# Performance work log

Hardware: AMD Instinct MI355X
Metric: run time of the kernel (lower is better)

The kernel has to match this reference:

```python
import jax, jax.numpy as jnp
import numpy as np

DIM = 1024
NUM_HEADS = 16
HEAD_DIM = DIM // NUM_HEADS
SCALE = HEAD_DIM ** -0.5


def rotate_half(x):
    x1, x2 = jnp.split(x, 2, axis=-1)
    return jnp.concatenate((-x2, x1), axis=-1)


def setup_inputs() -> dict:
    key = jax.random.key(0)
    ks = jax.random.split(key, 8)
    B, N = 2, 2048
    x = jax.random.normal(ks[0], (B, N, DIM), dtype=jnp.float32)
    # RoPE tables, broadcast over batch and heads
    pos = jnp.arange(N, dtype=jnp.float32)[:, None]
    inv_freq = 1.0 / (10000.0 ** (jnp.arange(0, HEAD_DIM, 2, dtype=jnp.float32) / HEAD_DIM))
    ang = pos * inv_freq[None, :]                       # [N, HEAD_DIM/2]
    ang = jnp.concatenate([ang, ang], axis=-1)          # [N, HEAD_DIM]
    rope_cos = jnp.cos(ang)[None, None]                 # [1,1,N,HEAD_DIM]
    rope_sin = jnp.sin(ang)[None, None]
    s = DIM ** -0.5
    qkv_w = jax.random.normal(ks[1], (3 * DIM, DIM), dtype=jnp.float32) * s
    qkv_b = jnp.zeros((3 * DIM,), dtype=jnp.float32)
    proj_w = jax.random.normal(ks[2], (DIM, DIM), dtype=jnp.float32) * s
    proj_b = jnp.zeros((DIM,), dtype=jnp.float32)
    return {"x": x, "rope_cos": rope_cos, "rope_sin": rope_sin,
            "qkv_w": qkv_w, "qkv_b": qkv_b, "proj_w": proj_w, "proj_b": proj_b}


def reference(x, rope_cos, rope_sin, qkv_w, qkv_b, proj_w, proj_b):
    B, N, C = x.shape
    H, D = NUM_HEADS, HEAD_DIM
    qkv = x @ qkv_w.T + qkv_b                            # [B,N,3C]
    qkv = qkv.reshape(B, N, 3, H, D).transpose(2, 0, 3, 1, 4)  # [3,B,H,N,D]
    q, k, v = qkv[0], qkv[1], qkv[2]
    # RoPE on q, k
    q = q * rope_cos + rotate_half(q) * rope_sin
    k = k * rope_cos + rotate_half(k) * rope_sin
    # scaled dot-product attention
    scores = jnp.einsum('bhnd,bhmd->bhnm', q, k) * SCALE
    attn = jax.nn.softmax(scores, axis=-1)
    out = jnp.einsum('bhnm,bhmd->bhnd', attn, v)         # [B,H,N,D]
    out = out.transpose(0, 2, 1, 3).reshape(B, N, C)
    return out @ proj_w.T + proj_b
```

## Files before the change

### kernel.cpp

```cpp
#include <hip/hip_runtime.h>
#include <hip/hip_bf16.h>

#define NUM_HEADS 16
#define HEAD_DIM 64
#define DIM 1024
#define NTOK 2048
#define MTOT 4096

typedef __attribute__((ext_vector_type(8))) short bf16x8;
typedef __attribute__((ext_vector_type(4))) float f32x4;
typedef __attribute__((ext_vector_type(16))) float f32x16;
typedef __attribute__((ext_vector_type(2))) unsigned int uint2v;

__device__ __forceinline__ unsigned short f2bf(float f) {
    union { __hip_bfloat16 h; unsigned short u; } c;
    c.h = __float2bfloat16(f);
    return c.u;
}

__device__ __forceinline__ unsigned int packbf(float lo, float hi) {
    union { unsigned short us[2]; unsigned int u; } p;
    p.us[0] = f2bf(lo); p.us[1] = f2bf(hi);
    return p.u;
}

__device__ __forceinline__ void plswap(unsigned int &a, unsigned int &b) {
#if __has_builtin(__builtin_amdgcn_permlane32_swap)
    uint2v r = __builtin_amdgcn_permlane32_swap(a, b, false, false);
    a = r[0]; b = r[1];
#else
    unsigned int pa = (unsigned int)__shfl_xor((int)a, 32);
    unsigned int pb = (unsigned int)__shfl_xor((int)b, 32);
    bool hi = (threadIdx.x & 32) != 0;
    unsigned int an = hi ? pb : a;
    unsigned int bn = hi ? b : pa;
    a = an; b = bn;
#endif
}

__device__ __forceinline__ void gload16(const unsigned short* g, unsigned short* l) {
    __builtin_amdgcn_global_load_lds(
        (const __attribute__((address_space(1))) void*)g,
        (__attribute__((address_space(3))) void*)l, 16, 0, 0);
}

__global__ __launch_bounds__(256) void k_conv3(
    const float* __restrict__ s0, unsigned short* __restrict__ d0, int n0,
    const float* __restrict__ s1, unsigned short* __restrict__ d1, int n1,
    const float* __restrict__ s2, unsigned short* __restrict__ d2, int n2)
{
    int blk = blockIdx.x;
    int b0 = n0 >> 11, b1 = n1 >> 11;
    const float* s; unsigned short* d; int i;
    if (blk < b0)            { s = s0; d = d0; i = blk; }
    else if (blk < b0 + b1)  { s = s1; d = d1; i = blk - b0; }
    else                     { s = s2; d = d2; i = blk - b0 - b1; }
    int idx = (i * 256 + threadIdx.x) * 8;
    float4 a = *(const float4*)(s + idx);
    float4 b = *(const float4*)(s + idx + 4);
    union { unsigned short us[8]; uint4 u4; } p;
    p.us[0] = f2bf(a.x); p.us[1] = f2bf(a.y); p.us[2] = f2bf(a.z); p.us[3] = f2bf(a.w);
    p.us[4] = f2bf(b.x); p.us[5] = f2bf(b.y); p.us[6] = f2bf(b.z); p.us[7] = f2bf(b.w);
    *(uint4*)(d + idx) = p.u4;
}

__global__ __launch_bounds__(256) void k_gemm_qkv(
    const unsigned short* __restrict__ xb, const unsigned short* __restrict__ wb,
    const float* __restrict__ bias, const float* __restrict__ rcos,
    const float* __restrict__ rsin,
    unsigned short* __restrict__ qb, unsigned short* __restrict__ kb,
    unsigned short* __restrict__ vtb)
{
    __shared__ __align__(16) unsigned char smem[34816];
    unsigned short* As = (unsigned short*)smem;
    unsigned short* Bs = (unsigned short*)(smem + 16384);

    const int tid  = threadIdx.x;
    const int lane = tid & 63;
    const int wid  = tid >> 6;
    const int lr   = lane & 15;
    const int g    = lane >> 4;
    const int wm   = (wid >> 1) * 64;
    const int wn   = (wid & 1) * 64;
    const int m0   = blockIdx.x * 128;
    const int n0   = blockIdx.y * 128;

    f32x4 acc[4][4];
    #pragma unroll
    for (int i = 0; i < 4; ++i)
        #pragma unroll
        for (int j = 0; j < 4; ++j) acc[i][j] = (f32x4){0.f, 0.f, 0.f, 0.f};

    for (int k0 = 0; k0 < DIM; k0 += 64) {
        #pragma unroll
        for (int it = 0; it < 4; ++it) {
            int p   = tid + it * 256;
            int row = p >> 3;
            int c   = (p & 7) ^ (row & 7);
            gload16(xb + (size_t)(m0 + row) * DIM + k0 + c*8, As + p*8);
            gload16(wb + (size_t)(n0 + row) * DIM + k0 + c*8, Bs + p*8);
        }
        __syncthreads();
        #pragma unroll
        for (int kk = 0; kk < 2; ++kk) {
            bf16x8 af[4], bfr[4];
            #pragma unroll
            for (int i = 0; i < 4; ++i) {
                int row = wm + i*16 + lr;
                af[i] = *(const bf16x8*)(As + row*64 + (((kk*4 + g) ^ (row & 7)) << 3));
            }
            #pragma unroll
            for (int j = 0; j < 4; ++j) {
                int row = wn + j*16 + lr;
                bfr[j] = *(const bf16x8*)(Bs + row*64 + (((kk*4 + g) ^ (row & 7)) << 3));
            }
            #pragma unroll
            for (int i = 0; i < 4; ++i)
                #pragma unroll
                for (int j = 0; j < 4; ++j)
                    acc[i][j] = __builtin_amdgcn_mfma_f32_16x16x32_bf16(af[i], bfr[j], acc[i][j], 0, 0, 0);
        }
        __syncthreads();
    }

    const int sect = n0 >> 10;
    float bq[4];
    #pragma unroll
    for (int j = 0; j < 4; ++j) bq[j] = bias[n0 + wn + j*16 + lr];

    if (sect < 2) {
        unsigned short* dst = sect ? kb : qb;
        const float sc = sect ? 1.0f : 0.125f * 1.44269504088896f;
        const int h = ((n0 & 1023) + wn) >> 6;
        #pragma unroll
        for (int i = 0; i < 4; ++i) {
            #pragma unroll
            for (int v = 0; v < 4; ++v) {
                int gm = m0 + wm + i*16 + g*4 + v;
                int b  = gm >> 11, n = gm & 2047;
                size_t base = ((size_t)(b*NUM_HEADS + h) * NTOK + n) << 6;
                #pragma unroll
                for (int j = 0; j < 4; ++j) {
                    int d = j*16 + lr;
                    float val = acc[i][j][v] + bq[j];
                    float vp  = acc[i][j^2][v] + bq[j^2];
                    float rot = (j < 2) ? -vp : vp;
                    float c = rcos[n*64 + d], s = rsin[n*64 + d];
                    dst[base + d] = f2bf((val * c + rot * s) * sc);
                }
            }
        }
    } else {
        unsigned short (*vt)[136] = (unsigned short (*)[136])smem;
        __syncthreads();
        #pragma unroll
        for (int i = 0; i < 4; ++i)
            #pragma unroll
            for (int j = 0; j < 4; ++j)
                #pragma unroll
                for (int v = 0; v < 4; ++v) {
                    int row = wm + i*16 + g*4 + v;
                    int c   = wn + j*16 + lr;
                    vt[c][row] = f2bf(acc[i][j][v] + bq[j]);
                }
        __syncthreads();
        const int b = m0 >> 11;
        const int nbase = m0 & 2047;
        #pragma unroll
        for (int it = 0; it < 8; ++it) {
            int c   = (tid >> 4) + it * 16;
            int sc2 = (n0 & 1023) + c;
            int hh  = sc2 >> 6, d = sc2 & 63;
            int nloc = (tid & 15) * 8;
            uint4 val = *(uint4*)&vt[c][nloc];
            *(uint4*)(vtb + ((size_t)(b*NUM_HEADS + hh) * HEAD_DIM + d) * NTOK + nbase + nloc) = val;
        }
    }
}

__global__ __launch_bounds__(256, 2) void k_attn(
    const unsigned short* __restrict__ qb, const unsigned short* __restrict__ kb,
    const unsigned short* __restrict__ vtb, unsigned short* __restrict__ attnb)
{
    __shared__ __align__(16) char sb[32768];

    const int tid  = threadIdx.x;
    const int lane = tid & 63;
    const int w    = tid >> 6;
    const int hi   = lane >> 5;
    const int lc   = lane & 31;
    const int q0   = blockIdx.x * 128;
    const int bh   = blockIdx.y;
    const int b    = bh >> 4, h = bh & 15;

    int kfoff[2][4], vfoff[2][4];
    #pragma unroll
    for (int s = 0; s < 2; ++s)
        #pragma unroll
        for (int ks = 0; ks < 4; ++ks) {
            int row = 32*s + lc;
            kfoff[s][ks] = row*128 + (((2*ks + hi) ^ (row & 7)) << 4);
            vfoff[s][ks] = 16384 + row*128 + (((2*ks + hi) ^ (row & 7)) << 4);
        }

    const unsigned short* gk[2];
    const unsigned short* gv[2];
    char* dk[2]; char* dv[2];
    {
        const unsigned short* kbase = kb  + (size_t)bh * NTOK * 64;
        const unsigned short* vbase = vtb + (size_t)bh * HEAD_DIM * NTOK;
        #pragma unroll
        for (int hp = 0; hp < 2; ++hp) {
            int p   = tid + hp * 256;
            int row = p >> 3;
            int c   = (p & 7) ^ (row & 7);
            gk[hp] = kbase + row*64 + c*8;
            gv[hp] = vbase + (size_t)row*NTOK + c*8;
            dk[hp] = sb + p*16;
            dv[hp] = sb + 16384 + p*16;
        }
    }

    bf16x8 qa[4];
    {
        size_t qrow = ((size_t)bh * NTOK + q0 + w*32 + lc) * 64;
        #pragma unroll
        for (int ks = 0; ks < 4; ++ks)
            qa[ks] = *(const bf16x8*)(qb + qrow + ks*16 + hi*8);
    }

    const f32x16 z16 = {0.f,0.f,0.f,0.f, 0.f,0.f,0.f,0.f, 0.f,0.f,0.f,0.f, 0.f,0.f,0.f,0.f};
    f32x16 o2[2];
    o2[0] = z16; o2[1] = z16;
    float m_ = -1e30f, lsum = 0.f;

    #pragma unroll
    for (int hp = 0; hp < 2; ++hp) {
        gload16(gk[hp], (unsigned short*)dk[hp]);
        gload16(gv[hp], (unsigned short*)dv[hp]);
        gk[hp] += 4096; gv[hp] += 64;
    }
    __syncthreads();

#define ATTN_ITER(X, DO_STAGE)                                                   \
    {                                                                            \
        if (DO_STAGE) {                                                          \
            _Pragma("unroll")                                                    \
            for (int hp = 0; hp < 2; ++hp) {                                     \
                gload16(gk[hp], (unsigned short*)(dk[hp] + ((X) ^ 8192)));       \
                gload16(gv[hp], (unsigned short*)(dv[hp] + ((X) ^ 8192)));       \
                gk[hp] += 4096; gv[hp] += 64;                                    \
            }                                                                    \
        }                                                                        \
                                          \
        f32x16 S0, S1;                                                           \
        {                                                                        \
            bf16x8 kf0[4], kf1[4];                                               \
            _Pragma("unroll")                                                    \
            for (int ks = 0; ks < 4; ++ks) {                                     \
                kf0[ks] = *(const bf16x8*)(sb + kfoff[0][ks] + (X));             \
                kf1[ks] = *(const bf16x8*)(sb + kfoff[1][ks] + (X));             \
            }                                                                    \
            __builtin_amdgcn_s_setprio(1);                                       \
            S0 = __builtin_amdgcn_mfma_f32_32x32x16_bf16(kf0[0], qa[0], z16, 0, 0, 0); \
            S1 = __builtin_amdgcn_mfma_f32_32x32x16_bf16(kf1[0], qa[0], z16, 0, 0, 0); \
            _Pragma("unroll")                                                    \
            for (int ks = 1; ks < 4; ++ks) {                                     \
                S0 = __builtin_amdgcn_mfma_f32_32x32x16_bf16(kf0[ks], qa[ks], S0, 0, 0, 0); \
                S1 = __builtin_amdgcn_mfma_f32_32x32x16_bf16(kf1[ks], qa[ks], S1, 0, 0, 0); \
            }                                                                    \
            __builtin_amdgcn_s_setprio(0);                                       \
        }                                                                        \
                          \
        float t[16];                                                             \
        _Pragma("unroll")                                                        \
        for (int r = 0; r < 16; ++r) t[r] = fmaxf(S0[r], S1[r]);                 \
        _Pragma("unroll")                                                        \
        for (int st = 8; st > 0; st >>= 1)                                       \
            _Pragma("unroll")                                                    \
            for (int i = 0; i < 8; ++i) if (i < st) t[i] = fmaxf(t[i], t[i + st]); \
        float lmax = t[0];                                                       \
        if (__any(lmax > m_ + 8.f)) {                                            \
            float mx = fmaxf(lmax, __shfl_xor(lmax, 32));                        \
            float mn = fmaxf(m_, mx);                                            \
            float scl = __builtin_amdgcn_exp2f(m_ - mn);                         \
            m_ = mn;                                                             \
            lsum *= scl;                                                         \
            o2[0] *= scl; o2[1] *= scl;                                          \
        }                                                                        \
                                               \
        _Pragma("unroll")                                                        \
        for (int r = 0; r < 16; ++r) {                                           \
            S0[r] = __builtin_amdgcn_exp2f(S0[r] - m_);                          \
            S1[r] = __builtin_amdgcn_exp2f(S1[r] - m_);                          \
        }                                                                        \
        _Pragma("unroll")                                                        \
        for (int r = 0; r < 16; ++r) t[r] = S0[r] + S1[r];                       \
        _Pragma("unroll")                                                        \
        for (int st = 8; st > 0; st >>= 1)                                       \
            _Pragma("unroll")                                                    \
            for (int i = 0; i < 8; ++i) if (i < st) t[i] += t[i + st];           \
        lsum += t[0];                                                            \
                \
        unsigned int dwA[2][4], dwB[2][4];                                       \
        _Pragma("unroll")                                                        \
        for (int c = 0; c < 4; ++c) {                                            \
            dwA[0][c] = packbf(S0[4*c],     S0[4*c + 1]);                        \
            dwB[0][c] = packbf(S0[4*c + 2], S0[4*c + 3]);                        \
            dwA[1][c] = packbf(S1[4*c],     S1[4*c + 1]);                        \
            dwB[1][c] = packbf(S1[4*c + 2], S1[4*c + 3]);                        \
        }                                                                        \
        bf16x8 pB[4];                                                            \
        _Pragma("unroll")                                                        \
        for (int t16 = 0; t16 < 4; ++t16) {                                      \
            int s = t16 >> 1, u = t16 & 1;                                       \
            unsigned int a0 = dwA[s][2*u], b0 = dwA[s][2*u + 1];                 \
            unsigned int a1 = dwB[s][2*u], b1 = dwB[s][2*u + 1];                 \
            plswap(a0, b0);                                                      \
            plswap(a1, b1);                                                      \
            union { unsigned int u4[4]; bf16x8 v; } pk;                          \
            pk.u4[0] = a0; pk.u4[1] = a1; pk.u4[2] = b0; pk.u4[3] = b1;          \
            pB[t16] = pk.v;                                                      \
        }                                                                        \
                             \
        _Pragma("unroll")                                                        \
        for (int t16 = 0; t16 < 4; ++t16) {                                      \
            bf16x8 vf0 = *(const bf16x8*)(sb + vfoff[0][t16] + (X));             \
            bf16x8 vf1 = *(const bf16x8*)(sb + vfoff[1][t16] + (X));             \
            __builtin_amdgcn_s_setprio(1);                                       \
            o2[0] = __builtin_amdgcn_mfma_f32_32x32x16_bf16(vf0, pB[t16], o2[0], 0, 0, 0); \
            o2[1] = __builtin_amdgcn_mfma_f32_32x32x16_bf16(vf1, pB[t16], o2[1], 0, 0, 0); \
            __builtin_amdgcn_s_setprio(0);                                       \
        }                                                                        \
        __syncthreads();                                                         \
    }

    #pragma unroll 1
    for (int tt = 0; tt < NTOK/64; tt += 2) {
        ATTN_ITER(0,    true);
        ATTN_ITER(8192, (tt + 2 < NTOK/64));
    }
#undef ATTN_ITER

    lsum += __shfl_xor(lsum, 32);
    const float inv = 1.0f / lsum;
    const size_t obase = ((size_t)(b*NTOK + q0 + w*32 + lc)) * DIM + h*HEAD_DIM + hi*4;
    #pragma unroll
    for (int sd = 0; sd < 2; ++sd)
        #pragma unroll
        for (int c = 0; c < 4; ++c) {
            union { unsigned short us[4]; uint2 u2; } pk4;
            #pragma unroll
            for (int v = 0; v < 4; ++v) pk4.us[v] = f2bf(o2[sd][4*c + v] * inv);
            *(uint2*)(attnb + obase + sd*32 + c*8) = pk4.u2;
        }
}

__global__ __launch_bounds__(256) void k_proj(
    const unsigned short* __restrict__ a, const unsigned short* __restrict__ wb,
    const float* __restrict__ bias, float* __restrict__ out)
{
    __shared__ __align__(16) unsigned short As[8192];
    __shared__ __align__(16) unsigned short Bs[4096];

    const int tid  = threadIdx.x;
    const int lane = tid & 63;
    const int wid  = tid >> 6;
    const int lr   = lane & 15;
    const int g    = lane >> 4;
    const int wm   = (wid & 1) * 64;
    const int wn   = (wid >> 1) * 32;
    const int m0   = blockIdx.x * 128;
    const int n0   = blockIdx.y * 64;

    f32x4 acc[4][2];
    #pragma unroll
    for (int i = 0; i < 4; ++i)
        #pragma unroll
        for (int j = 0; j < 2; ++j) acc[i][j] = (f32x4){0.f, 0.f, 0.f, 0.f};

    for (int k0 = 0; k0 < DIM; k0 += 64) {
        #pragma unroll
        for (int it = 0; it < 4; ++it) {
            int p   = tid + it * 256;
            int row = p >> 3;
            int c   = (p & 7) ^ (row & 7);
            gload16(a + (size_t)(m0 + row) * DIM + k0 + c*8, As + p*8);
        }
        #pragma unroll
        for (int it = 0; it < 2; ++it) {
            int p   = tid + it * 256;
            int row = p >> 3;
            int c   = (p & 7) ^ (row & 7);
            gload16(wb + (size_t)(n0 + row) * DIM + k0 + c*8, Bs + p*8);
        }
        __syncthreads();
        #pragma unroll
        for (int kk = 0; kk < 2; ++kk) {
            bf16x8 af[4], bfr[2];
            #pragma unroll
            for (int i = 0; i < 4; ++i) {
                int row = wm + i*16 + lr;
                af[i] = *(const bf16x8*)(As + row*64 + (((kk*4 + g) ^ (row & 7)) << 3));
            }
            #pragma unroll
            for (int j = 0; j < 2; ++j) {
                int row = wn + j*16 + lr;
                bfr[j] = *(const bf16x8*)(Bs + row*64 + (((kk*4 + g) ^ (row & 7)) << 3));
            }
            #pragma unroll
            for (int i = 0; i < 4; ++i)
                #pragma unroll
                for (int j = 0; j < 2; ++j)
                    acc[i][j] = __builtin_amdgcn_mfma_f32_16x16x32_bf16(af[i], bfr[j], acc[i][j], 0, 0, 0);
        }
        __syncthreads();
    }

    #pragma unroll
    for (int i = 0; i < 4; ++i)
        #pragma unroll
        for (int j = 0; j < 2; ++j)
            #pragma unroll
            for (int v = 0; v < 4; ++v) {
                int row = m0 + wm + i*16 + g*4 + v;
                int col = n0 + wn + j*16 + lr;
                out[(size_t)row * DIM + col] = acc[i][j][v] + bias[col];
            }
}

extern "C" void kernel_launch(void* const* d_in, const int* in_sizes, int n_in,
                              void* d_out, int out_size, void* d_ws, size_t ws_size,
                              hipStream_t stream)
{
    const float* x      = (const float*)d_in[0];
    const float* rcos   = (const float*)d_in[1];
    const float* rsin   = (const float*)d_in[2];
    const float* qkv_w  = (const float*)d_in[3];
    const float* qkv_b  = (const float*)d_in[4];
    const float* proj_w = (const float*)d_in[5];
    const float* proj_b = (const float*)d_in[6];
    float* out = (float*)d_out;

    const size_t BUF = (size_t)2 * NUM_HEADS * NTOK * HEAD_DIM;
    unsigned short* qb    = (unsigned short*)d_ws;
    unsigned short* kb    = qb + BUF;
    unsigned short* vtb   = kb + BUF;
    unsigned short* attnb = vtb + BUF;
    unsigned short* xbf   = attnb + BUF;
    unsigned short* wqkvb = xbf + (size_t)MTOT * DIM;
    unsigned short* wprjb = wqkvb + (size_t)3 * DIM * DIM;

    const int n0 = MTOT * DIM, n1 = 3 * DIM * DIM, n2 = DIM * DIM;
    k_conv3<<<dim3((n0 + n1 + n2) / 2048), 256, 0, stream>>>(
        x, xbf, n0, qkv_w, wqkvb, n1, proj_w, wprjb, n2);

    k_gemm_qkv<<<dim3(32, 24), 256, 0, stream>>>(xbf, wqkvb, qkv_b, rcos, rsin, qb, kb, vtb);
    k_attn<<<dim3(NTOK/128, 32), 256, 0, stream>>>(qb, kb, vtb, attnb);
    k_proj<<<dim3(32, 16), 256, 0, stream>>>(attnb, wprjb, proj_b, out);
}
```

Before: 121.5 us.

## Double KV tile to 128 keys and compute softmax row sums via MFMA

The attention kernel now processes 128 keys per iteration instead of 64, doubling the shared-memory K/V double buffer to 64KB. The V tile layout is changed to 256-byte rows with a 16-way XOR swizzle. Row sums of the softmax probabilities are now computed with an extra MFMA against a ones vector instead of a register reduction tree. The aim is fewer barriers and iterations and less VALU reduction work, at the cost of 64KB LDS per block, which may limit blocks per CU, and one extra MFMA per PV step.

```diff
diff --git a/kernel.cpp b/kernel.cpp
--- a/kernel.cpp
+++ b/kernel.cpp
@@ -182,7 +182,7 @@
     const unsigned short* __restrict__ qb, const unsigned short* __restrict__ kb,
     const unsigned short* __restrict__ vtb, unsigned short* __restrict__ attnb)
 {
-    __shared__ __align__(16) char sb[32768];
+    __shared__ __align__(16) char sb[65536];
 
     const int tid  = threadIdx.x;
     const int lane = tid & 63;
@@ -193,31 +193,32 @@
     const int bh   = blockIdx.y;
     const int b    = bh >> 4, h = bh & 15;
 
-    int kfoff[2][4], vfoff[2][4];
-    #pragma unroll
-    for (int s = 0; s < 2; ++s)
-        #pragma unroll
-        for (int ks = 0; ks < 4; ++ks) {
-            int row = 32*s + lc;
-            kfoff[s][ks] = row*128 + (((2*ks + hi) ^ (row & 7)) << 4);
-            vfoff[s][ks] = 16384 + row*128 + (((2*ks + hi) ^ (row & 7)) << 4);
-        }
-
-    const unsigned short* gk[2];
-    const unsigned short* gv[2];
-    char* dk[2]; char* dv[2];
+    int krow[4], kpart[4], vpart[8];
+    #pragma unroll
+    for (int s = 0; s < 4; ++s) krow[s] = (32*s + lc) * 128;
+    #pragma unroll
+    for (int ks = 0; ks < 4; ++ks) kpart[ks] = ((2*ks + hi) ^ (lc & 7)) << 4;
+    #pragma unroll
+    for (int t16 = 0; t16 < 8; ++t16) vpart[t16] = ((2*t16 + hi) ^ (lc & 15)) << 4;
+    const int vrow = lc * 256;
+
+    const unsigned short* gk[4];
+    const unsigned short* gv[4];
+    char* dk[4]; char* dv[4];
     {
         const unsigned short* kbase = kb  + (size_t)bh * NTOK * 64;
         const unsigned short* vbase = vtb + (size_t)bh * HEAD_DIM * NTOK;
         #pragma unroll
-        for (int hp = 0; hp < 2; ++hp) {
-            int p   = tid + hp * 256;
-            int row = p >> 3;
-            int c   = (p & 7) ^ (row & 7);
-            gk[hp] = kbase + row*64 + c*8;
-            gv[hp] = vbase + (size_t)row*NTOK + c*8;
-            dk[hp] = sb + p*16;
-            dv[hp] = sb + 16384 + p*16;
+        for (int it = 0; it < 4; ++it) {
+            int p  = tid + it * 256;
+            int kr = p >> 3;
+            int kc = (p & 7) ^ (kr & 7);
+            gk[it] = kbase + kr*64 + kc*8;
+            dk[it] = sb + p*16;
+            int vr = p >> 4;
+            int vc = (p & 15) ^ (vr & 15);
+            gv[it] = vbase + (size_t)vr*NTOK + vc*8;
+            dv[it] = sb + 32768 + p*16;
         }
     }
 
@@ -230,15 +231,20 @@
     }
 
     const f32x16 z16 = {0.f,0.f,0.f,0.f, 0.f,0.f,0.f,0.f, 0.f,0.f,0.f,0.f, 0.f,0.f,0.f,0.f};
+    bf16x8 onesa;
+    #pragma unroll
+    for (int j = 0; j < 8; ++j) onesa[j] = (short)0x3F80;
+
     f32x16 o2[2];
     o2[0] = z16; o2[1] = z16;
-    float m_ = -1e30f, lsum = 0.f;
-
-    #pragma unroll
-    for (int hp = 0; hp < 2; ++hp) {
-        gload16(gk[hp], (unsigned short*)dk[hp]);
-        gload16(gv[hp], (unsigned short*)dv[hp]);
-        gk[hp] += 4096; gv[hp] += 64;
+    f32x16 ol = z16;
+    float m_ = -1e30f;
+
+    #pragma unroll
+    for (int it = 0; it < 4; ++it) {
+        gload16(gk[it], (unsigned short*)dk[it]);
+        gload16(gv[it], (unsigned short*)dv[it]);
+        gk[it] += 8192; gv[it] += 128;
     }
     __syncthreads();
 
@@ -246,88 +252,72 @@
     {                                                                            \
         if (DO_STAGE) {                                                          \
             _Pragma("unroll")                                                    \
-            for (int hp = 0; hp < 2; ++hp) {                                     \
-                gload16(gk[hp], (unsigned short*)(dk[hp] + ((X) ^ 8192)));       \
-                gload16(gv[hp], (unsigned short*)(dv[hp] + ((X) ^ 8192)));       \
-                gk[hp] += 4096; gv[hp] += 64;                                    \
+            for (int it = 0; it < 4; ++it) {                                     \
+                gload16(gk[it], (unsigned short*)(dk[it] + ((X) ^ 16384)));      \
+                gload16(gv[it], (unsigned short*)(dv[it] + ((X) ^ 16384)));      \
+                gk[it] += 8192; gv[it] += 128;                                   \
             }                                                                    \
         }                                                                        \
-                                          \
-        f32x16 S0, S1;                                                           \
-        {                                                                        \
-            bf16x8 kf0[4], kf1[4];                                               \
-            _Pragma("unroll")                                                    \
-            for (int ks = 0; ks < 4; ++ks) {                                     \
-                kf0[ks] = *(const bf16x8*)(sb + kfoff[0][ks] + (X));             \
-                kf1[ks] = *(const bf16x8*)(sb + kfoff[1][ks] + (X));             \
-            }                                                                    \
-            __builtin_amdgcn_s_setprio(1);                                       \
-            S0 = __builtin_amdgcn_mfma_f32_32x32x16_bf16(kf0[0], qa[0], z16, 0, 0, 0); \
-            S1 = __builtin_amdgcn_mfma_f32_32x32x16_bf16(kf1[0], qa[0], z16, 0, 0, 0); \
+                        \
+        f32x16 S[4];                                                             \
+        __builtin_amdgcn_s_setprio(1);                                           \
+        _Pragma("unroll")                                                        \
+        for (int s = 0; s < 4; ++s) {                                            \
+            bf16x8 kf0 = *(const bf16x8*)(sb + (X) + krow[s] + kpart[0]);        \
+            S[s] = __builtin_amdgcn_mfma_f32_32x32x16_bf16(kf0, qa[0], z16, 0, 0, 0); \
             _Pragma("unroll")                                                    \
             for (int ks = 1; ks < 4; ++ks) {                                     \
-                S0 = __builtin_amdgcn_mfma_f32_32x32x16_bf16(kf0[ks], qa[ks], S0, 0, 0, 0); \
-                S1 = __builtin_amdgcn_mfma_f32_32x32x16_bf16(kf1[ks], qa[ks], S1, 0, 0, 0); \
+                bf16x8 kf = *(const bf16x8*)(sb + (X) + krow[s] + kpart[ks]);    \
+                S[s] = __builtin_amdgcn_mfma_f32_32x32x16_bf16(kf, qa[ks], S[s], 0, 0, 0); \
             }                                                                    \
-            __builtin_amdgcn_s_setprio(0);                                       \
         }                                                                        \
-                          \
-        float t[16];                                                             \
-        _Pragma("unroll")                                                        \
-        for (int r = 0; r < 16; ++r) t[r] = fmaxf(S0[r], S1[r]);                 \
+        __builtin_amdgcn_s_setprio(0);                                           \
+                                        \
+        float a_[16];                                                            \
+        _Pragma("unroll")                                                        \
+        for (int r = 0; r < 16; ++r)                                             \
+            a_[r] = fmaxf(fmaxf(S[0][r], S[1][r]), fmaxf(S[2][r], S[3][r]));     \
         _Pragma("unroll")                                                        \
         for (int st = 8; st > 0; st >>= 1)                                       \
             _Pragma("unroll")                                                    \
-            for (int i = 0; i < 8; ++i) if (i < st) t[i] = fmaxf(t[i], t[i + st]); \
-        float lmax = t[0];                                                       \
+            for (int i = 0; i < 8; ++i) if (i < st) a_[i] = fmaxf(a_[i], a_[i + st]); \
+        float lmax = a_[0];                                                      \
         if (__any(lmax > m_ + 8.f)) {                                            \
             float mx = fmaxf(lmax, __shfl_xor(lmax, 32));                        \
             float mn = fmaxf(m_, mx);                                            \
             float scl = __builtin_amdgcn_exp2f(m_ - mn);                         \
             m_ = mn;                                                             \
-            lsum *= scl;                                                         \
+            ol[0] *= scl;                                                        \
             o2[0] *= scl; o2[1] *= scl;                                          \
         }                                                                        \
-                                               \
-        _Pragma("unroll")                                                        \
-        for (int r = 0; r < 16; ++r) {                                           \
-            S0[r] = __builtin_amdgcn_exp2f(S0[r] - m_);                          \
-            S1[r] = __builtin_amdgcn_exp2f(S1[r] - m_);                          \
-        }                                                                        \
-        _Pragma("unroll")                                                        \
-        for (int r = 0; r < 16; ++r) t[r] = S0[r] + S1[r];                       \
-        _Pragma("unroll")                                                        \
-        for (int st = 8; st > 0; st >>= 1)                                       \
+                                                            \
+        _Pragma("unroll")                                                        \
+        for (int s = 0; s < 4; ++s)                                              \
             _Pragma("unroll")                                                    \
-            for (int i = 0; i < 8; ++i) if (i < st) t[i] += t[i + st];           \
-        lsum += t[0];                                                            \
+            for (int r = 0; r < 16; ++r)                                         \
+                S[s][r] = __builtin_amdgcn_exp2f(S[s][r] - m_);                  \
                 \
-        unsigned int dwA[2][4], dwB[2][4];                                       \
-        _Pragma("unroll")                                                        \
-        for (int c = 0; c < 4; ++c) {                                            \
-            dwA[0][c] = packbf(S0[4*c],     S0[4*c + 1]);                        \
-            dwB[0][c] = packbf(S0[4*c + 2], S0[4*c + 3]);                        \
-            dwA[1][c] = packbf(S1[4*c],     S1[4*c + 1]);                        \
-            dwB[1][c] = packbf(S1[4*c + 2], S1[4*c + 3]);                        \
-        }                                                                        \
-        bf16x8 pB[4];                                                            \
-        _Pragma("unroll")                                                        \
-        for (int t16 = 0; t16 < 4; ++t16) {                                      \
+        bf16x8 pB[8];                                                            \
+        _Pragma("unroll")                                                        \
+        for (int t16 = 0; t16 < 8; ++t16) {                                      \
             int s = t16 >> 1, u = t16 & 1;                                       \
-            unsigned int a0 = dwA[s][2*u], b0 = dwA[s][2*u + 1];                 \
-            unsigned int a1 = dwB[s][2*u], b1 = dwB[s][2*u + 1];                 \
+            unsigned int a0 = packbf(S[s][8*u],     S[s][8*u + 1]);              \
+            unsigned int b0 = packbf(S[s][8*u + 4], S[s][8*u + 5]);              \
+            unsigned int a1 = packbf(S[s][8*u + 2], S[s][8*u + 3]);              \
+            unsigned int b1 = packbf(S[s][8*u + 6], S[s][8*u + 7]);              \
             plswap(a0, b0);                                                      \
             plswap(a1, b1);                                                      \
             union { unsigned int u4[4]; bf16x8 v; } pk;                          \
             pk.u4[0] = a0; pk.u4[1] = a1; pk.u4[2] = b0; pk.u4[3] = b1;          \
             pB[t16] = pk.v;                                                      \
         }                                                                        \
-                             \
-        _Pragma("unroll")                                                        \
-        for (int t16 = 0; t16 < 4; ++t16) {                                      \
-            bf16x8 vf0 = *(const bf16x8*)(sb + vfoff[0][t16] + (X));             \
-            bf16x8 vf1 = *(const bf16x8*)(sb + vfoff[1][t16] + (X));             \
+                                                        \
+        _Pragma("unroll")                                                        \
+        for (int t16 = 0; t16 < 8; ++t16) {                                      \
+            bf16x8 vf0 = *(const bf16x8*)(sb + 32768 + (X) + vrow + vpart[t16]);         \
+            bf16x8 vf1 = *(const bf16x8*)(sb + 32768 + 8192 + (X) + vrow + vpart[t16]);  \
             __builtin_amdgcn_s_setprio(1);                                       \
+            ol    = __builtin_amdgcn_mfma_f32_32x32x16_bf16(onesa, pB[t16], ol, 0, 0, 0); \
             o2[0] = __builtin_amdgcn_mfma_f32_32x32x16_bf16(vf0, pB[t16], o2[0], 0, 0, 0); \
             o2[1] = __builtin_amdgcn_mfma_f32_32x32x16_bf16(vf1, pB[t16], o2[1], 0, 0, 0); \
             __builtin_amdgcn_s_setprio(0);                                       \
@@ -336,14 +326,13 @@
     }
 
     #pragma unroll 1
-    for (int tt = 0; tt < NTOK/64; tt += 2) {
-        ATTN_ITER(0,    true);
-        ATTN_ITER(8192, (tt + 2 < NTOK/64));
+    for (int tt = 0; tt < NTOK/128; tt += 2) {
+        ATTN_ITER(0,     true);
+        ATTN_ITER(16384, (tt + 2 < NTOK/128));
     }
 #undef ATTN_ITER
 
-    lsum += __shfl_xor(lsum, 32);
-    const float inv = 1.0f / lsum;
+    const float inv = 1.0f / ol[0];
     const size_t obase = ((size_t)(b*NTOK + q0 + w*32 + lc)) * DIM + h*HEAD_DIM + hi*4;
     #pragma unroll
     for (int sd = 0; sd < 2; ++sd)
```

Result: no change. 122.1 us (+0.5%).
